# Optimization experiments

Hardware: AMD Instinct MI355X
Metric: run time of the kernel (lower is better)

## Reference

```python
import jax, jax.numpy as jnp
import numpy as np

EPS = 1e-5
NUM_HEADS = 8
KEY_DEPTH = 128   # base_filters * key_expansion
VAL_DEPTH = 256   # base_filters * value_expansion
C_IN = 256


def conv1x1(x, w):
    # x: [N, Cin, L], w: [Cout, Cin] (1x1 conv, no bias)
    return jnp.einsum('oc,ncl->nol', w, x)


def group_norm1(x, w, b, eps=EPS):
    # torch GroupNorm(1, C) on [N, C, L]: normalize over (C, L) per sample,
    # per-channel affine.
    mu = jnp.mean(x, axis=(1, 2), keepdims=True)
    var = jnp.var(x, axis=(1, 2), keepdims=True)
    xn = (x - mu) * jax.lax.rsqrt(var + eps)
    return xn * w[None, :, None] + b[None, :, None]


def layer_norm_last2(x, eps=EPS):
    # freshly-constructed nn.LayerNorm([A, B]): weight=1, bias=0 -> pure norm
    mu = jnp.mean(x, axis=(-2, -1), keepdims=True)
    var = jnp.var(x, axis=(-2, -1), keepdims=True)
    return (x - mu) * jax.lax.rsqrt(var + eps)


def gelu(x):
    return jax.nn.gelu(x, approximate=False)  # torch F.gelu default (erf)


def setup_inputs() -> dict:
    key = jax.random.key(0)
    ks = jax.random.split(key, 16)
    N, L = 8, 1024
    qkv_out = 2 * KEY_DEPTH + VAL_DEPTH  # 512

    def w(k, shape, std=0.02):
        return jax.random.normal(k, shape, jnp.float32) * std

    def gw(k, c):
        return 1.0 + 0.1 * jax.random.normal(k, (c,), jnp.float32)

    return {
        'f': jax.random.normal(ks[0], (N, C_IN, L), jnp.float32),
        'w_z': w(ks[1], (C_IN, C_IN), np.sqrt(2.0 / C_IN)),
        'gz_w': gw(ks[2], C_IN), 'gz_b': w(ks[3], (C_IN,)),
        'w_qkv': w(ks[4], (qkv_out, C_IN), C_IN ** -0.5),
        'gq_w': gw(ks[5], qkv_out), 'gq_b': w(ks[6], (qkv_out,)),
        'w_out': w(ks[7], (C_IN, VAL_DEPTH), np.sqrt(2.0 / VAL_DEPTH)),
        'go_w': gw(ks[8], C_IN), 'go_b': w(ks[9], (C_IN,)),
        'w_ffn1': w(ks[10], (2 * C_IN, C_IN), np.sqrt(2.0 / C_IN)),
        'g1_w': gw(ks[11], 2 * C_IN), 'g1_b': w(ks[12], (2 * C_IN,)),
        'w_ffn2': w(ks[13], (C_IN, 2 * C_IN), np.sqrt(1.0 / C_IN)),
        'g2_w': gw(ks[14], C_IN), 'g2_b': w(ks[15], (C_IN,)),
    }


def reference(f, w_z, gz_w, gz_b, w_qkv, gq_w, gq_b, w_out, go_w, go_b,
              w_ffn1, g1_w, g1_b, w_ffn2, g2_w, g2_b):
    N, C, L = f.shape
    H = NUM_HEADS

    z = gelu(group_norm1(conv1x1(gelu(f), w_z), gz_w, gz_b))
    qkv = group_norm1(conv1x1(z, w_qkv), gq_w, gq_b)
    q, k, v = jnp.split(qkv, [KEY_DEPTH, 2 * KEY_DEPTH], axis=1)
    q = q.reshape(N, H, KEY_DEPTH // H, L)
    k = k.reshape(N, H, KEY_DEPTH // H, L)
    v = v.reshape(N, H, VAL_DEPTH // H, L)

    # [N, H, L, L] similarity, no scaling, then LayerNorm over full LxL map
    logits = jnp.einsum('nhcl,nhcm->nhlm', q, k)
    logits = layer_norm_last2(logits)

    # scatter-mask: diagonal -> -inf for every head
    eye = jnp.eye(L, dtype=bool)[None, None]  # [1,1,L,L]
    logits = jnp.where(eye, -jnp.inf, logits)

    attn = jax.nn.softmax(logits.astype(jnp.float32), axis=-1)
    attn = jnp.where(jnp.isnan(attn), 0.0, attn)

    out = jnp.einsum('nhlm,nhdm->nhdl', attn, v).reshape(N, VAL_DEPTH, L)
    out = gelu(layer_norm_last2(out))  # LayerNorm([C_v, L]), fresh params

    out = group_norm1(conv1x1(out, w_out), go_w, go_b)
    f = gelu(f + out)

    h = gelu(group_norm1(conv1x1(f, w_ffn1), g1_w, g1_b))
    h = group_norm1(conv1x1(h, w_ffn2), g2_w, g2_b)
    return gelu(f + h)
```

## Files before the change

### kernel.cpp

```cpp
#include <hip/hip_runtime.h>

#define LSEQ 1024

typedef __attribute__((ext_vector_type(8))) short bf16x8;
typedef __attribute__((ext_vector_type(4))) float f32x4;

__device__ __forceinline__ float gelu_f(float x){
    return 0.5f*x*(1.0f+erff(x*0.7071067811865476f));
}

__device__ __forceinline__ unsigned cvtpk(float lo, float hi){
    unsigned r;
    asm("v_cvt_pk_bf16_f32 %0, %1, %2" : "=v"(r) : "v"(lo), "v"(hi));
    return r;
}

__global__ __launch_bounds__(256,2) void prologue(
    const float* __restrict__ w0, const float* __restrict__ w1,
    const float* __restrict__ w2, const float* __restrict__ w3,
    const float* __restrict__ w4, unsigned short* __restrict__ wdst,
    const float* __restrict__ f, unsigned short* __restrict__ t0,
    float* __restrict__ stats, float* __restrict__ covs,
    unsigned* __restrict__ kmaxu)
{
    __shared__ float T[64][68];
    int b = blockIdx.x;
    int tid = threadIdx.x;

    if(b < 512){
        int ltile = (b&15)*64, ctile = ((b>>4)&3)*64, n = b>>6;
        const float* s = f + (size_t)n*256*LSEQ;
        int cl = tid>>4, l4 = (tid&15)*4;
        #pragma unroll
        for(int p=0;p<4;p++){
            int c_loc = p*16 + cl;
            float4 v = *(const float4*)&s[(size_t)(ctile+c_loc)*LSEQ + ltile + l4];
            float4 t;
            t.x = gelu_f(v.x); t.y = gelu_f(v.y); t.z = gelu_f(v.z); t.w = gelu_f(v.w);
            *(float4*)&T[c_loc][l4] = t;
        }
        __syncthreads();
        int l_loc = tid>>2, cg = (tid&3)*16;
        uint4 o0, o1;
        o0.x = cvtpk(T[cg+0][l_loc],  T[cg+1][l_loc]);
        o0.y = cvtpk(T[cg+2][l_loc],  T[cg+3][l_loc]);
        o0.z = cvtpk(T[cg+4][l_loc],  T[cg+5][l_loc]);
        o0.w = cvtpk(T[cg+6][l_loc],  T[cg+7][l_loc]);
        o1.x = cvtpk(T[cg+8][l_loc],  T[cg+9][l_loc]);
        o1.y = cvtpk(T[cg+10][l_loc], T[cg+11][l_loc]);
        o1.z = cvtpk(T[cg+12][l_loc], T[cg+13][l_loc]);
        o1.w = cvtpk(T[cg+14][l_loc], T[cg+15][l_loc]);
        unsigned short* d = t0 + (size_t)n*LSEQ*256 + (size_t)(ltile+l_loc)*256 + ctile + cg;
        *(uint4*)d = o0;
        *(uint4*)(d+8) = o1;
    } else if(b < 1024){
        int idx4 = (b-512)*256 + tid;
        const float* src; int off4;
        if(idx4 < 16384){ src=w0; off4=idx4; }
        else if(idx4 < 49152){ src=w1; off4=idx4-16384; }
        else if(idx4 < 65536){ src=w2; off4=idx4-49152; }
        else if(idx4 < 98304){ src=w3; off4=idx4-65536; }
        else { src=w4; off4=idx4-98304; }
        float4 v = ((const float4*)src)[off4];
        uint2 p; p.x = cvtpk(v.x,v.y); p.y = cvtpk(v.z,v.w);
        ((uint2*)wdst)[idx4] = p;
    } else if(b == 1024){
        if(tid < 64) ((float4*)stats)[tid] = (float4){0.f,0.f,0.f,0.f};
        if(tid >= 64 && tid < 80) ((uint4*)kmaxu)[tid-64] = (uint4){0,0,0,0};
    } else {
        int i = (b-1025)*256 + tid;
        ((float4*)covs)[i] = (float4){0.f,0.f,0.f,0.f};
    }
}

__global__ __launch_bounds__(256,2) void xform_bf16(
    const float* __restrict__ src, const float* __restrict__ res,
    const float* __restrict__ stats,
    const float* __restrict__ gw, const float* __restrict__ gb,
    float cnt_inv, int C, unsigned short* __restrict__ dst)
{
    __shared__ float T[64][68];
    int n = blockIdx.z;
    int ltile = blockIdx.x*64, ctile = blockIdx.y*64;
    int tid = threadIdx.x;

    float mu=0.f, istd=1.f;
    if(stats){
        float s1 = stats[2*n], s2 = stats[2*n+1];
        mu = s1*cnt_inv;
        istd = rsqrtf(s2*cnt_inv - mu*mu + 1e-5f);
    }
    const float* s = src + (size_t)n*C*LSEQ;
    const float* r = res ? res + (size_t)n*C*LSEQ : nullptr;

    int cl = tid>>4, l4 = (tid&15)*4;
    #pragma unroll
    for(int p=0;p<4;p++){
        int c_loc = p*16 + cl;
        int c = ctile + c_loc;
        float w_ = 1.f, b_ = 0.f;
        if(stats){ w_ = istd; b_ = -mu*istd; }
        if(gw){ b_ = gb[c] + b_*gw[c]; w_ *= gw[c]; }
        float4 v = *(const float4*)&s[(size_t)c*LSEQ + ltile + l4];
        float4 t;
        t.x = v.x*w_+b_; t.y = v.y*w_+b_; t.z = v.z*w_+b_; t.w = v.w*w_+b_;
        if(r){
            float4 rv = *(const float4*)&r[(size_t)c*LSEQ + ltile + l4];
            t.x += rv.x; t.y += rv.y; t.z += rv.z; t.w += rv.w;
        }
        t.x = gelu_f(t.x); t.y = gelu_f(t.y); t.z = gelu_f(t.z); t.w = gelu_f(t.w);
        *(float4*)&T[c_loc][l4] = t;
    }
    __syncthreads();

    int l_loc = tid>>2, cg = (tid&3)*16;
    uint4 o0, o1;
    o0.x = cvtpk(T[cg+0][l_loc],  T[cg+1][l_loc]);
    o0.y = cvtpk(T[cg+2][l_loc],  T[cg+3][l_loc]);
    o0.z = cvtpk(T[cg+4][l_loc],  T[cg+5][l_loc]);
    o0.w = cvtpk(T[cg+6][l_loc],  T[cg+7][l_loc]);
    o1.x = cvtpk(T[cg+8][l_loc],  T[cg+9][l_loc]);
    o1.y = cvtpk(T[cg+10][l_loc], T[cg+11][l_loc]);
    o1.z = cvtpk(T[cg+12][l_loc], T[cg+13][l_loc]);
    o1.w = cvtpk(T[cg+14][l_loc], T[cg+15][l_loc]);
    unsigned short* d = dst + (size_t)n*LSEQ*C + (size_t)(ltile+l_loc)*C + ctile + cg;
    *(uint4*)d = o0;
    *(uint4*)(d+8) = o1;
}

__global__ __launch_bounds__(256,2) void gemm_bf16(
    const unsigned short* __restrict__ Abf,
    const unsigned short* __restrict__ Bbf,
    float* __restrict__ C,
    int M, int K,
    float* __restrict__ out_stats)
{
    __shared__ short As[64*264];
    __shared__ short Bs[64*264];

    int tid = threadIdx.x;
    int n = blockIdx.z, n0 = blockIdx.x*64, m0 = blockIdx.y*64;
    int wave = tid>>6, lane = tid&63;
    int col = lane&15, quad = lane>>4;
    int srow = tid>>2, sks = (tid&3)*8;

    const unsigned short* apt = Abf + (size_t)(m0+srow)*K + sks;
    const unsigned short* bpt = Bbf + ((size_t)n*LSEQ + n0+srow)*K + sks;

    f32x4 acc[4];
    #pragma unroll
    for(int t=0;t<4;t++) acc[t] = (f32x4){0.f,0.f,0.f,0.f};

    for(int kp=0; kp<K; kp+=256){
        __syncthreads();
        uint4 av[8], bw[8];
        #pragma unroll
        for(int i=0;i<8;i++) av[i] = *(const uint4*)(apt + kp + i*32);
        #pragma unroll
        for(int i=0;i<8;i++) bw[i] = *(const uint4*)(bpt + kp + i*32);
        #pragma unroll
        for(int i=0;i<8;i++) *(uint4*)&As[srow*264 + sks + i*32] = av[i];
        #pragma unroll
        for(int i=0;i<8;i++) *(uint4*)&Bs[srow*264 + sks + i*32] = bw[i];
        __syncthreads();

        #pragma unroll
        for(int kc=0;kc<8;kc++){
            bf16x8 af = *(bf16x8*)&As[(wave*16+col)*264 + kc*32 + quad*8];
            #pragma unroll
            for(int t=0;t<4;t++){
                bf16x8 bf = *(bf16x8*)&Bs[(t*16+col)*264 + kc*32 + quad*8];
                acc[t] = __builtin_amdgcn_mfma_f32_16x16x32_bf16(af, bf, acc[t], 0,0,0);
            }
        }
    }

    __syncthreads();
    size_t cbase = (size_t)n*M*LSEQ;
    float lsum=0.f, lsq=0.f;
    #pragma unroll
    for(int t=0;t<4;t++){
        #pragma unroll
        for(int r2=0;r2<4;r2++){
            int m = m0 + wave*16 + quad*4 + r2;
            int l = n0 + t*16 + col;
            float v = acc[t][r2];
            C[cbase + (size_t)m*LSEQ + l] = v;
            lsum += v; lsq += v*v;
        }
    }
    float* scr = (float*)As;
    scr[tid] = lsum; scr[256+tid] = lsq;
    __syncthreads();
    for(int s=128;s>0;s>>=1){
        if(tid<s){ scr[tid]+=scr[tid+s]; scr[256+tid]+=scr[256+tid+s]; }
        __syncthreads();
    }
    if(tid==0){
        atomicAdd(&out_stats[2*n],   scr[0]);
        atomicAdd(&out_stats[2*n+1], scr[256]);
    }
}

__global__ __launch_bounds__(256,2) void head_cov(
    const float* __restrict__ qkv,
    const float* __restrict__ s_qkv,
    const float* __restrict__ gq_w, const float* __restrict__ gq_b,
    float* __restrict__ covq, float* __restrict__ covk,
    float* __restrict__ sumq, float* __restrict__ sumk,
    unsigned short* __restrict__ Qbf, unsigned short* __restrict__ Kbf,
    unsigned short* __restrict__ Vbf,
    float* __restrict__ qnorm, unsigned* __restrict__ kmaxu)
{
    __shared__ float Kq[16*132];
    __shared__ float Kk[16*132];
    int b = blockIdx.x;
    int head = b>>3, chunk = b&7;
    int n = head>>3, h = head&7;
    int tid = threadIdx.x;
    int m0 = chunk*128;

    float s1 = s_qkv[2*n], s2v = s_qkv[2*n+1];
    float mu  = s1*(1.f/524288.f);
    float var = s2v*(1.f/524288.f) - mu*mu;
    float istd = rsqrtf(var + 1e-5f);

    const float* base = qkv + (size_t)n*512*LSEQ;
    int m = tid&127, cg = tid>>7;
    #pragma unroll
    for(int cc=0;cc<8;cc++){
        int c = cg*8+cc;
        int chq = h*16+c, chk = 128+h*16+c;
        Kq[c*132+m] = (base[(size_t)chq*LSEQ+m0+m]-mu)*istd*gq_w[chq]+gq_b[chq];
        Kk[c*132+m] = (base[(size_t)chk*LSEQ+m0+m]-mu)*istd*gq_w[chk]+gq_b[chk];
    }

    {
        int d = tid>>3, mg = tid&7;
        int ch = 256 + h*32 + d;
        float vw = gq_w[ch]*istd, vb = gq_b[ch]-mu*istd*gq_w[ch];
        const float* vs = base + (size_t)ch*LSEQ + m0 + mg*16;
        float4 a0 = *(const float4*)&vs[0];
        float4 a1 = *(const float4*)&vs[4];
        float4 a2 = *(const float4*)&vs[8];
        float4 a3 = *(const float4*)&vs[12];
        uint4 p0, p1;
        p0.x = cvtpk(a0.x*vw+vb, a0.y*vw+vb);
        p0.y = cvtpk(a0.z*vw+vb, a0.w*vw+vb);
        p0.z = cvtpk(a1.x*vw+vb, a1.y*vw+vb);
        p0.w = cvtpk(a1.z*vw+vb, a1.w*vw+vb);
        p1.x = cvtpk(a2.x*vw+vb, a2.y*vw+vb);
        p1.y = cvtpk(a2.z*vw+vb, a2.w*vw+vb);
        p1.z = cvtpk(a3.x*vw+vb, a3.y*vw+vb);
        p1.w = cvtpk(a3.z*vw+vb, a3.w*vw+vb);
        unsigned short* dv = Vbf + ((size_t)head*32 + d)*1024 + m0 + mg*16;
        *(uint4*)dv = p0;
        *(uint4*)(dv+8) = p1;
    }
    __syncthreads();

    int i = tid>>4, j = tid&15;
    float q0=0,q1=0,q2=0,q3=0, k0=0,k1=0,k2=0,k3=0;
    for(int mm=0;mm<128;mm+=4){
        float4 qa = *(const float4*)&Kq[i*132+mm];
        float4 qb = *(const float4*)&Kq[j*132+mm];
        q0 += qa.x*qb.x; q1 += qa.y*qb.y; q2 += qa.z*qb.z; q3 += qa.w*qb.w;
        float4 ka = *(const float4*)&Kk[i*132+mm];
        float4 kb = *(const float4*)&Kk[j*132+mm];
        k0 += ka.x*kb.x; k1 += ka.y*kb.y; k2 += ka.z*kb.z; k3 += ka.w*kb.w;
    }
    atomicAdd(&covq[head*256 + i*16 + j], (q0+q1)+(q2+q3));
    atomicAdd(&covk[head*256 + i*16 + j], (k0+k1)+(k2+k3));

    if(i==0){
        float s=0.f;
        for(int mm=0;mm<128;mm+=4){
            float4 v = *(const float4*)&Kq[j*132+mm];
            s += (v.x+v.y)+(v.z+v.w);
        }
        atomicAdd(&sumq[head*16+j], s);
    }
    if(i==1){
        float s=0.f;
        for(int mm=0;mm<128;mm+=4){
            float4 v = *(const float4*)&Kk[j*132+mm];
            s += (v.x+v.y)+(v.z+v.w);
        }
        atomicAdd(&sumk[head*16+j], s);
    }

    {
        int mm2 = tid & 127;
        if(tid < 128){
            unsigned u[8]; float s2 = 0.f;
            #pragma unroll
            for(int c=0;c<16;c+=2){
                float a = Kq[c*132+mm2], b2 = Kq[(c+1)*132+mm2];
                s2 += a*a + b2*b2;
                u[c>>1] = cvtpk(a, b2);
            }
            unsigned short* dq = Qbf + ((size_t)head*1024 + m0 + mm2)*16;
            *(uint4*)dq     = *(uint4*)&u[0];
            *(uint4*)(dq+8) = *(uint4*)&u[4];
            qnorm[head*1024 + m0 + mm2] = s2;
        } else {
            unsigned u[8]; float s2 = 0.f;
            #pragma unroll
            for(int c=0;c<16;c+=2){
                float a = Kk[c*132+mm2], b2 = Kk[(c+1)*132+mm2];
                s2 += a*a + b2*b2;
                u[c>>1] = cvtpk(a, b2);
            }
            unsigned short* dk = Kbf + ((size_t)head*1024 + m0 + mm2)*16;
            *(uint4*)dk     = *(uint4*)&u[0];
            *(uint4*)(dk+8) = *(uint4*)&u[4];
            #pragma unroll
            for(int d=1;d<64;d<<=1) s2 = fmaxf(s2, __shfl_xor(s2, d));
            if((tid&63)==0) atomicMax(kmaxu + head, __float_as_uint(s2));
        }
    }
}

__global__ __launch_bounds__(256) void attn_kernel(
    const unsigned short* __restrict__ Qbf,
    const unsigned short* __restrict__ Kbf,
    const unsigned short* __restrict__ Vbf,
    const float* __restrict__ qnorm, const unsigned* __restrict__ kmaxu,
    const float* __restrict__ covq, const float* __restrict__ covk,
    const float* __restrict__ sumq, const float* __restrict__ sumk,
    float* __restrict__ out,
    float* __restrict__ out_stats)
{
    __shared__ short Qs[64*40];
    __shared__ short Ks[128*40];
    __shared__ short Vs[32*136];
    __shared__ short Ps[64*152];
    __shared__ float bounds_l[64];
    __shared__ float issum_l[64];
    __shared__ float sred4[4];

    int b = blockIdx.x;
    int head = b&63, rb = b>>6;
    int n = head>>3, h = head&7;
    int tid = threadIdx.x;
    int wv = tid>>6, lane = tid&63;
    int col = lane&15, quad = lane>>4;
    int l0 = rb*64;

    float ih;
    {
        float prod = covq[head*256+tid]*covk[head*256+tid];
        #pragma unroll
        for(int d=1;d<64;d<<=1) prod += __shfl_xor(prod, d);
        if(lane==0) sred4[wv] = prod;
        __syncthreads();
        if(tid==0){
            double S2 = (double)sred4[0] + (double)sred4[1]
                      + (double)sred4[2] + (double)sred4[3];
            double S1 = 0.0;
            for(int c=0;c<16;c++)
                S1 += (double)sumq[head*16+c]*(double)sumk[head*16+c];
            double cnt = 1048576.0;
            double mean = S1/cnt;
            double v2 = S2/cnt - mean*mean;
            if(v2 < 0.0) v2 = 0.0;
            sred4[0] = (float)(1.0/sqrt(v2 + 1e-5));
        }
        __syncthreads();
        ih = sred4[0];
    }
    float ihl = ih * 1.4426950408889634f;

    {
        uint4 z = {0,0,0,0};
        int row = tid>>1, hf = tid&1;
        *(uint4*)&Ks[row*40 + 16 + hf*8] = z;
        if(row < 64) *(uint4*)&Qs[row*40 + 16 + hf*8] = z;
        if(tid < 64){
            const unsigned short* qsrc = Qbf + ((size_t)head*1024 + l0 + tid)*16;
            *(uint4*)&Qs[tid*40]     = *(const uint4*)qsrc;
            *(uint4*)&Qs[tid*40 + 8] = *(const uint4*)(qsrc + 8);
            bounds_l[tid] = sqrtf(qnorm[head*1024 + l0 + tid]);
        }
    }
    float kmax = sqrtf(__uint_as_float(kmaxu[head]));
    __syncthreads();

    int rl = wv*16 + col;
    bf16x8 qf = *(bf16x8*)&Qs[rl*40 + quad*8];
    float B2l = bounds_l[rl]*kmax*ihl;
    int grow = l0 + rl;

    int krow = tid>>1, khalf = tid&1;
    const unsigned short* ksrc = Kbf + ((size_t)head*1024 + krow)*16 + khalf*8;
    int vdd = tid>>3, vmg = tid&7;
    const unsigned short* vsrc = Vbf + ((size_t)head*32 + vdd)*1024 + vmg*16;

    f32x4 acc[2];
    acc[0]=(f32x4){0,0,0,0}; acc[1]=(f32x4){0,0,0,0};
    float ssum = 0.f;
    const f32x4 zero4 = {0.f,0.f,0.f,0.f};

    uint4 kreg = *(const uint4*)ksrc;
    uint4 vr0  = *(const uint4*)vsrc;
    uint4 vr1  = *(const uint4*)(vsrc + 8);

    int diag_mc = rb>>1;
    for(int mc=0;mc<8;mc++){
        int M0 = mc*128;
        *(uint4*)&Ks[krow*40 + khalf*8]  = kreg;
        *(uint4*)&Vs[vdd*136 + vmg*16]     = vr0;
        *(uint4*)&Vs[vdd*136 + vmg*16 + 8] = vr1;
        __syncthreads();

        if(mc < 7){
            kreg = *(const uint4*)(ksrc + (size_t)(M0+128)*16);
            vr0  = *(const uint4*)(vsrc + M0+128);
            vr1  = *(const uint4*)(vsrc + M0+136);
        }

        __builtin_amdgcn_s_setprio(1);
        bool dg = (mc == diag_mc);
        #pragma unroll
        for(int mt=0;mt<8;mt++){
            bf16x8 ak = *(bf16x8*)&Ks[(mt*16+col)*40 + quad*8];
            f32x4 sc = __builtin_amdgcn_mfma_f32_16x16x32_bf16(ak, qf, zero4, 0,0,0);
            float pr[4];
            #pragma unroll
            for(int r=0;r<4;r++)
                pr[r] = exp2f(fmaf(sc[r], ihl, -B2l));
            if(dg){
                int mbase = M0 + mt*16 + quad*4;
                #pragma unroll
                for(int r=0;r<4;r++)
                    if(mbase + r == grow) pr[r] = 0.f;
            }
            ssum += (pr[0]+pr[1])+(pr[2]+pr[3]);
            uint2 pw;
            pw.x = cvtpk(pr[0],pr[1]); pw.y = cvtpk(pr[2],pr[3]);
            *(uint2*)&Ps[rl*152 + mt*16 + quad*4] = pw;
        }
        #pragma unroll
        for(int kk=0;kk<4;kk++){
            bf16x8 bv0 = *(bf16x8*)&Vs[( col)*136 + kk*32 + quad*8];
            bf16x8 bv1 = *(bf16x8*)&Vs[(16+col)*136 + kk*32 + quad*8];
            bf16x8 ap = *(bf16x8*)&Ps[rl*152 + kk*32 + quad*8];
            acc[0] = __builtin_amdgcn_mfma_f32_16x16x32_bf16(ap, bv0, acc[0], 0,0,0);
            acc[1] = __builtin_amdgcn_mfma_f32_16x16x32_bf16(ap, bv1, acc[1], 0,0,0);
        }
        __builtin_amdgcn_s_setprio(0);
        __syncthreads();
    }

    {
        float v = ssum;
        v += __shfl_xor(v,16);
        v += __shfl_xor(v,32);
        if(quad==0) issum_l[rl] = v;
    }
    __syncthreads();
    if(tid<64) issum_l[tid] = 1.f/issum_l[tid];
    __syncthreads();

    float* ep = (float*)Ps;
    #pragma unroll
    for(int dt=0;dt<2;dt++)
        *(f32x4*)&ep[(dt*16+col)*68 + wv*16 + quad*4] = acc[dt];
    __syncthreads();

    float lsum=0.f, lsq=0.f;
    size_t obase = (size_t)n*262144 + (size_t)h*32*LSEQ + l0;
    #pragma unroll
    for(int t=0;t<8;t++){
        int idx = t*256 + tid;
        int d = idx>>6, row = idx&63;
        float y = ep[d*68+row]*issum_l[row];
        out[obase + (size_t)d*LSEQ + row] = y;
        lsum += y; lsq += y*y;
    }
    float* red = (float*)Ks;
    red[tid]=lsum; red[256+tid]=lsq;
    __syncthreads();
    for(int s=128;s>0;s>>=1){
        if(tid<s){ red[tid]+=red[tid+s]; red[256+tid]+=red[256+tid+s]; }
        __syncthreads();
    }
    if(tid==0){
        atomicAdd(&out_stats[2*n],   red[0]);
        atomicAdd(&out_stats[2*n+1], red[256]);
    }
}

__global__ __launch_bounds__(256) void ew_final(
    const float* __restrict__ f, const float* __restrict__ x,
    const float* __restrict__ h2,
    const float* __restrict__ sx, const float* __restrict__ sh,
    const float* __restrict__ go_w, const float* __restrict__ go_b,
    const float* __restrict__ g2_w, const float* __restrict__ g2_b,
    float* __restrict__ out)
{
    int idx = blockIdx.x*256 + threadIdx.x;
    int n = idx >> 16;
    int c = (idx >> 8) & 255;
    float mux, isx, muh, ish;
    {
        float s1 = sx[2*n], s2 = sx[2*n+1];
        mux = s1*(1.f/262144.f);
        isx = rsqrtf(s2*(1.f/262144.f) - mux*mux + 1e-5f);
        float t1 = sh[2*n], t2 = sh[2*n+1];
        muh = t1*(1.f/262144.f);
        ish = rsqrtf(t2*(1.f/262144.f) - muh*muh + 1e-5f);
    }
    float wo = go_w[c]*isx, bo = go_b[c]-mux*isx*go_w[c];
    float w2 = g2_w[c]*ish, b2 = g2_b[c]-muh*ish*g2_w[c];
    float4 xv = ((const float4*)x)[idx];
    float4 fv = ((const float4*)f)[idx];
    float4 hv = ((const float4*)h2)[idx];
    float4 ov;
    float f1;
    f1 = gelu_f(fv.x + xv.x*wo+bo); ov.x = gelu_f(f1 + hv.x*w2+b2);
    f1 = gelu_f(fv.y + xv.y*wo+bo); ov.y = gelu_f(f1 + hv.y*w2+b2);
    f1 = gelu_f(fv.z + xv.z*wo+bo); ov.z = gelu_f(f1 + hv.z*w2+b2);
    f1 = gelu_f(fv.w + xv.w*wo+bo); ov.w = gelu_f(f1 + hv.w*w2+b2);
    ((float4*)out)[idx] = ov;
}

extern "C" void kernel_launch(void* const* d_in, const int* in_sizes, int n_in,
                              void* d_out, int out_size, void* d_ws, size_t ws_size,
                              hipStream_t stream) {
    const float* f     = (const float*)d_in[0];
    const float* w_z   = (const float*)d_in[1];
    const float* gz_w  = (const float*)d_in[2];
    const float* gz_b  = (const float*)d_in[3];
    const float* w_qkv = (const float*)d_in[4];
    const float* gq_w  = (const float*)d_in[5];
    const float* gq_b  = (const float*)d_in[6];
    const float* w_out = (const float*)d_in[7];
    const float* go_w  = (const float*)d_in[8];
    const float* go_b  = (const float*)d_in[9];
    const float* w_f1  = (const float*)d_in[10];
    const float* g1_w  = (const float*)d_in[11];
    const float* g1_b  = (const float*)d_in[12];
    const float* w_f2  = (const float*)d_in[13];
    const float* g2_w  = (const float*)d_in[14];
    const float* g2_b  = (const float*)d_in[15];

    float* ws = (float*)d_ws;
    float* stats = ws;
    float* s_z    = stats + 0;
    float* s_qkv  = stats + 16;
    float* s_attn = stats + 32;
    float* s_x    = stats + 48;
    float* s_h1   = stats + 64;
    float* s_h2   = stats + 80;

    float* qkvF = ws + 256;
    float* z0F  = qkvF + 4194304;
    float* xF   = z0F + 2097152;
    unsigned short* t0 = (unsigned short*)(xF + 2097152);
    unsigned short* t1 = t0 + 2097152;
    unsigned short* wp = t1 + 2097152;
    unsigned short* t4 = (unsigned short*)z0F;
    unsigned short* wp_z   = wp;
    unsigned short* wp_qkv = wp + 65536;
    unsigned short* wp_out = wp + 196608;
    unsigned short* wp_f1  = wp + 262144;
    unsigned short* wp_f2  = wp + 393216;

    float* covq = xF;
    float* covk = xF + 16384;
    float* sumq = xF + 32768;
    float* sumk = xF + 33792;
    float* qnorm = xF + 34816;
    unsigned* kmaxu = (unsigned*)(xF + 100352);

    unsigned short* Qbf = t0;
    unsigned short* Kbf = t0 + 1048576;
    unsigned short* Vbf = t1;

    float* outp = (float*)d_out;

    dim3 blk(256);
    prologue<<<1059,blk,0,stream>>>(w_z, w_qkv, w_out, w_f1, w_f2, wp,
        f, t0, stats, covq, kmaxu);
    gemm_bf16<<<dim3(16,4,8),blk,0,stream>>>(wp_z, t0, z0F, 256, 256, s_z);
    xform_bf16<<<dim3(16,4,8),blk,0,stream>>>(z0F, nullptr, s_z, gz_w, gz_b,
        1.f/262144.f, 256, t1);
    gemm_bf16<<<dim3(16,8,8),blk,0,stream>>>(wp_qkv, t1, qkvF, 512, 256, s_qkv);
    head_cov<<<512,blk,0,stream>>>(qkvF, s_qkv, gq_w, gq_b, covq, covk, sumq, sumk,
        Qbf, Kbf, Vbf, qnorm, kmaxu);
    attn_kernel<<<1024,blk,0,stream>>>(Qbf, Kbf, Vbf, qnorm, kmaxu,
        covq, covk, sumq, sumk, z0F, s_attn);
    xform_bf16<<<dim3(16,4,8),blk,0,stream>>>(z0F, nullptr, s_attn, nullptr, nullptr,
        1.f/262144.f, 256, t0);
    gemm_bf16<<<dim3(16,4,8),blk,0,stream>>>(wp_out, t0, xF, 256, 256, s_x);
    xform_bf16<<<dim3(16,4,8),blk,0,stream>>>(xF, f, s_x, go_w, go_b,
        1.f/262144.f, 256, t1);
    gemm_bf16<<<dim3(16,8,8),blk,0,stream>>>(wp_f1, t1, qkvF, 512, 256, s_h1);
    xform_bf16<<<dim3(16,8,8),blk,0,stream>>>(qkvF, nullptr, s_h1, g1_w, g1_b,
        1.f/524288.f, 512, t4);
    gemm_bf16<<<dim3(16,4,8),blk,0,stream>>>(wp_f2, t4, qkvF, 256, 512, s_h2);
    ew_final<<<2048,blk,0,stream>>>(f, xF, qkvF, s_x, s_h2,
        go_w, go_b, g2_w, g2_b, outp);
}
```

Before: 312.2 us.

## Process 128 query rows per attention block to reuse K/V tiles

The attention kernel now handles 128 query rows per block instead of 64, with each wave computing two 16-row tiles against every staged K/V chunk. The grid is halved to 512 blocks. The goal is to halve global K/V loads and LDS staging per query row, and to amortize the per-block setup and barriers over more work. In exchange it uses more LDS (a larger P buffer) and more registers for the doubled accumulators, which may reduce occupancy, and fewer blocks means less parallelism across the GPU's CUs.

New measurement: 301.5 us. -3.4%, faster.

```diff
diff --git a/kernel.cpp b/kernel.cpp
--- a/kernel.cpp
+++ b/kernel.cpp
@@ -331,12 +331,12 @@
     float* __restrict__ out,
     float* __restrict__ out_stats)
 {
-    __shared__ short Qs[64*40];
+    __shared__ short Qs[128*40];
     __shared__ short Ks[128*40];
     __shared__ short Vs[32*136];
-    __shared__ short Ps[64*152];
-    __shared__ float bounds_l[64];
-    __shared__ float issum_l[64];
+    __shared__ short Ps[128*152];
+    __shared__ float bounds_l[128];
+    __shared__ float issum_l[128];
     __shared__ float sred4[4];
 
     int b = blockIdx.x;
@@ -345,7 +345,7 @@
     int tid = threadIdx.x;
     int wv = tid>>6, lane = tid&63;
     int col = lane&15, quad = lane>>4;
-    int l0 = rb*64;
+    int l0 = rb*128;
 
     float ih;
     {
@@ -375,40 +375,42 @@
         uint4 z = {0,0,0,0};
         int row = tid>>1, hf = tid&1;
         *(uint4*)&Ks[row*40 + 16 + hf*8] = z;
-        if(row < 64) *(uint4*)&Qs[row*40 + 16 + hf*8] = z;
-        if(tid < 64){
-            const unsigned short* qsrc = Qbf + ((size_t)head*1024 + l0 + tid)*16;
-            *(uint4*)&Qs[tid*40]     = *(const uint4*)qsrc;
-            *(uint4*)&Qs[tid*40 + 8] = *(const uint4*)(qsrc + 8);
-            bounds_l[tid] = sqrtf(qnorm[head*1024 + l0 + tid]);
-        }
+        *(uint4*)&Qs[row*40 + 16 + hf*8] = z;
+        const unsigned short* qsrc = Qbf + ((size_t)head*1024 + l0 + row)*16 + hf*8;
+        *(uint4*)&Qs[row*40 + hf*8] = *(const uint4*)qsrc;
+        if(tid < 128) bounds_l[tid] = sqrtf(qnorm[head*1024 + l0 + tid]);
     }
     float kmax = sqrtf(__uint_as_float(kmaxu[head]));
     __syncthreads();
 
-    int rl = wv*16 + col;
-    bf16x8 qf = *(bf16x8*)&Qs[rl*40 + quad*8];
-    float B2l = bounds_l[rl]*kmax*ihl;
-    int grow = l0 + rl;
+    bf16x8 qf[2];
+    float B2l[2]; int grow[2];
+    #pragma unroll
+    for(int t=0;t<2;t++){
+        int rl = (2*wv+t)*16 + col;
+        qf[t] = *(bf16x8*)&Qs[rl*40 + quad*8];
+        B2l[t] = bounds_l[rl]*kmax*ihl;
+        grow[t] = l0 + rl;
+    }
 
     int krow = tid>>1, khalf = tid&1;
     const unsigned short* ksrc = Kbf + ((size_t)head*1024 + krow)*16 + khalf*8;
     int vdd = tid>>3, vmg = tid&7;
     const unsigned short* vsrc = Vbf + ((size_t)head*32 + vdd)*1024 + vmg*16;
 
-    f32x4 acc[2];
-    acc[0]=(f32x4){0,0,0,0}; acc[1]=(f32x4){0,0,0,0};
-    float ssum = 0.f;
+    f32x4 acc[2][2];
+    #pragma unroll
+    for(int t=0;t<2;t++){ acc[t][0]=(f32x4){0,0,0,0}; acc[t][1]=(f32x4){0,0,0,0}; }
+    float ssum[2] = {0.f,0.f};
     const f32x4 zero4 = {0.f,0.f,0.f,0.f};
 
     uint4 kreg = *(const uint4*)ksrc;
     uint4 vr0  = *(const uint4*)vsrc;
     uint4 vr1  = *(const uint4*)(vsrc + 8);
 
-    int diag_mc = rb>>1;
     for(int mc=0;mc<8;mc++){
         int M0 = mc*128;
-        *(uint4*)&Ks[krow*40 + khalf*8]  = kreg;
+        *(uint4*)&Ks[krow*40 + khalf*8]    = kreg;
         *(uint4*)&Vs[vdd*136 + vmg*16]     = vr0;
         *(uint4*)&Vs[vdd*136 + vmg*16 + 8] = vr1;
         __syncthreads();
@@ -420,61 +422,70 @@
         }
 
         __builtin_amdgcn_s_setprio(1);
-        bool dg = (mc == diag_mc);
+        bool dg = (mc == rb);
         #pragma unroll
         for(int mt=0;mt<8;mt++){
             bf16x8 ak = *(bf16x8*)&Ks[(mt*16+col)*40 + quad*8];
-            f32x4 sc = __builtin_amdgcn_mfma_f32_16x16x32_bf16(ak, qf, zero4, 0,0,0);
-            float pr[4];
             #pragma unroll
-            for(int r=0;r<4;r++)
-                pr[r] = exp2f(fmaf(sc[r], ihl, -B2l));
-            if(dg){
-                int mbase = M0 + mt*16 + quad*4;
+            for(int t=0;t<2;t++){
+                f32x4 sc = __builtin_amdgcn_mfma_f32_16x16x32_bf16(ak, qf[t], zero4, 0,0,0);
+                float pr[4];
                 #pragma unroll
                 for(int r=0;r<4;r++)
-                    if(mbase + r == grow) pr[r] = 0.f;
+                    pr[r] = exp2f(fmaf(sc[r], ihl, -B2l[t]));
+                if(dg){
+                    int mbase = M0 + mt*16 + quad*4;
+                    #pragma unroll
+                    for(int r=0;r<4;r++)
+                        if(mbase + r == grow[t]) pr[r] = 0.f;
+                }
+                ssum[t] += (pr[0]+pr[1])+(pr[2]+pr[3]);
+                uint2 pw;
+                pw.x = cvtpk(pr[0],pr[1]); pw.y = cvtpk(pr[2],pr[3]);
+                *(uint2*)&Ps[((2*wv+t)*16+col)*152 + mt*16 + quad*4] = pw;
             }
-            ssum += (pr[0]+pr[1])+(pr[2]+pr[3]);
-            uint2 pw;
-            pw.x = cvtpk(pr[0],pr[1]); pw.y = cvtpk(pr[2],pr[3]);
-            *(uint2*)&Ps[rl*152 + mt*16 + quad*4] = pw;
         }
         #pragma unroll
         for(int kk=0;kk<4;kk++){
             bf16x8 bv0 = *(bf16x8*)&Vs[( col)*136 + kk*32 + quad*8];
             bf16x8 bv1 = *(bf16x8*)&Vs[(16+col)*136 + kk*32 + quad*8];
-            bf16x8 ap = *(bf16x8*)&Ps[rl*152 + kk*32 + quad*8];
-            acc[0] = __builtin_amdgcn_mfma_f32_16x16x32_bf16(ap, bv0, acc[0], 0,0,0);
-            acc[1] = __builtin_amdgcn_mfma_f32_16x16x32_bf16(ap, bv1, acc[1], 0,0,0);
+            #pragma unroll
+            for(int t=0;t<2;t++){
+                bf16x8 ap = *(bf16x8*)&Ps[((2*wv+t)*16+col)*152 + kk*32 + quad*8];
+                acc[t][0] = __builtin_amdgcn_mfma_f32_16x16x32_bf16(ap, bv0, acc[t][0], 0,0,0);
+                acc[t][1] = __builtin_amdgcn_mfma_f32_16x16x32_bf16(ap, bv1, acc[t][1], 0,0,0);
+            }
         }
         __builtin_amdgcn_s_setprio(0);
         __syncthreads();
     }
 
-    {
-        float v = ssum;
+    #pragma unroll
+    for(int t=0;t<2;t++){
+        float v = ssum[t];
         v += __shfl_xor(v,16);
         v += __shfl_xor(v,32);
-        if(quad==0) issum_l[rl] = v;
-    }
-    __syncthreads();
-    if(tid<64) issum_l[tid] = 1.f/issum_l[tid];
+        if(quad==0) issum_l[(2*wv+t)*16+col] = v;
+    }
+    __syncthreads();
+    if(tid<128) issum_l[tid] = 1.f/issum_l[tid];
     __syncthreads();
 
     float* ep = (float*)Ps;
     #pragma unroll
-    for(int dt=0;dt<2;dt++)
-        *(f32x4*)&ep[(dt*16+col)*68 + wv*16 + quad*4] = acc[dt];
+    for(int t=0;t<2;t++)
+        #pragma unroll
+        for(int dt=0;dt<2;dt++)
+            *(f32x4*)&ep[(dt*16+col)*132 + (2*wv+t)*16 + quad*4] = acc[t][dt];
     __syncthreads();
 
     float lsum=0.f, lsq=0.f;
     size_t obase = (size_t)n*262144 + (size_t)h*32*LSEQ + l0;
     #pragma unroll
-    for(int t=0;t<8;t++){
+    for(int t=0;t<16;t++){
         int idx = t*256 + tid;
-        int d = idx>>6, row = idx&63;
-        float y = ep[d*68+row]*issum_l[row];
+        int d = idx>>7, row = idx&127;
+        float y = ep[d*132+row]*issum_l[row];
         out[obase + (size_t)d*LSEQ + row] = y;
         lsum += y; lsq += y*y;
     }
@@ -589,7 +600,7 @@
     gemm_bf16<<<dim3(16,8,8),blk,0,stream>>>(wp_qkv, t1, qkvF, 512, 256, s_qkv);
     head_cov<<<512,blk,0,stream>>>(qkvF, s_qkv, gq_w, gq_b, covq, covk, sumq, sumk,
         Qbf, Kbf, Vbf, qnorm, kmaxu);
-    attn_kernel<<<1024,blk,0,stream>>>(Qbf, Kbf, Vbf, qnorm, kmaxu,
+    attn_kernel<<<512,blk,0,stream>>>(Qbf, Kbf, Vbf, qnorm, kmaxu,
         covq, covk, sumq, sumk, z0F, s_attn);
     xform_bf16<<<dim3(16,4,8),blk,0,stream>>>(z0F, nullptr, s_attn, nullptr, nullptr,
         1.f/262144.f, 256, t0);
```
